# Optimization experiments

Hardware: AMD Instinct MI355X
Metric: run time of the kernel (lower is better)

Reference implementation:

```python
import jax, jax.numpy as jnp
import numpy as np

B, T, C, H, D = 2, 2048, 1024, 16, 64

def setup_inputs() -> dict:
    key = jax.random.key(0)
    ks = jax.random.split(key, 5)
    s = 1.0 / np.sqrt(C)
    return {
        "hidden_states": jax.random.normal(ks[0], (B, T, C), jnp.float32),
        "Wq": jax.random.normal(ks[1], (H, C, D), jnp.float32) * s,
        "Wk": jax.random.normal(ks[2], (H, C, D), jnp.float32) * s,
        "Wv": jax.random.normal(ks[3], (H, C, D), jnp.float32) * s,
        "Wo": jax.random.normal(ks[4], (C, C), jnp.float32) * s,
    }

def reference(hidden_states, Wq, Wk, Wv, Wo):
    x = hidden_states  # (B, T, C)
    q = jnp.einsum("btc,hcd->bhtd", x, Wq)
    k = jnp.einsum("btc,hcd->bhtd", x, Wk)
    v = jnp.einsum("btc,hcd->bhtd", x, Wv)
    scale = 1.0 / jnp.sqrt(jnp.asarray(D, x.dtype))
    scores = jnp.einsum("bhtd,bhsd->bhts", q, k) * scale  # (B,H,T,T)
    Tlen = x.shape[1]
    causal = jnp.tril(jnp.ones((Tlen, Tlen), bool))
    scores = jnp.where(causal, scores, jnp.asarray(-jnp.inf, x.dtype))
    probs = jax.nn.softmax(scores, axis=-1)
    heads = jnp.einsum("bhts,bhsd->bhtd", probs, v)  # (B,H,T,D)
    concat = heads.transpose(0, 2, 1, 3).reshape(x.shape[0], Tlen, H * D)  # (B,T,C)
    return jnp.einsum("btc,oc->bto", concat, Wo)  # output projection (dropout=0)
```

## Files before the change

kernel.cpp:

```cpp
#include <hip/hip_runtime.h>
#include <math.h>

#define B_ 2
#define T_ 2048
#define C_ 1024
#define H_ 16
#define D_ 64

typedef short short8 __attribute__((ext_vector_type(8)));
typedef float f32x4 __attribute__((ext_vector_type(4)));

#define LOG2E 1.44269504088896f

__device__ __forceinline__ unsigned short f2bf(float f) {
    unsigned int u = __float_as_uint(f);
    u += 0x7FFFu + ((u >> 16) & 1u);
    return (unsigned short)(u >> 16);
}

#define NCAST 2560

__global__ __launch_bounds__(256) void prep_all(
    const float* __restrict__ x,  const float* __restrict__ Wq,
    const float* __restrict__ Wk, const float* __restrict__ Wv,
    const float* __restrict__ Wo,
    unsigned short* __restrict__ xb,   unsigned short* __restrict__ Wall,
    unsigned short* __restrict__ wob,  int nX, int nW)
{
    const int bid = blockIdx.x;
    const int tid = threadIdx.x;
    if (bid < NCAST) {
        int i = (bid * 256 + tid) * 8;
        const float* s;
        unsigned short* d;
        if (i < nX) { s = x + i; d = xb + i; }
        else {
            int j = i - nX;
            if (j >= nW) return;
            s = Wo + j; d = wob + j;
        }
        float4 a = *(const float4*)s;
        float4 b = *(const float4*)(s + 4);
        ushort4 o0, o1;
        o0.x = f2bf(a.x); o0.y = f2bf(a.y); o0.z = f2bf(a.z); o0.w = f2bf(a.w);
        o1.x = f2bf(b.x); o1.y = f2bf(b.y); o1.z = f2bf(b.z); o1.w = f2bf(b.w);
        *(ushort4*)d = o0;
        *(ushort4*)(d + 4) = o1;
        return;
    }
    __shared__ float t[64][65];
    const int tb = bid - NCAST;
    const int c0 = (tb & 15) * 64;
    const int h  = (tb >> 4) & 15;
    const int z  = tb >> 8;
    const float* W = (z == 0) ? Wq : (z == 1) ? Wk : Wv;
    unsigned short* Wt = Wall + (size_t)z * H_ * D_ * C_;
    const int r = tid >> 4, c4 = (tid & 15) * 4;
    #pragma unroll
    for (int p = 0; p < 4; p++) {
        int cl = r + p * 16;
        float4 v = *(const float4*)&W[((size_t)h * C_ + c0 + cl) * D_ + c4];
        t[cl][c4 + 0] = v.x; t[cl][c4 + 1] = v.y;
        t[cl][c4 + 2] = v.z; t[cl][c4 + 3] = v.w;
    }
    __syncthreads();
    #pragma unroll
    for (int p = 0; p < 4; p++) {
        int d = r + p * 16;
        ushort4 o;
        o.x = f2bf(t[c4 + 0][d]); o.y = f2bf(t[c4 + 1][d]);
        o.z = f2bf(t[c4 + 2][d]); o.w = f2bf(t[c4 + 3][d]);
        *(ushort4*)&Wt[((size_t)h * D_ + d) * C_ + c0 + c4] = o;
    }
}

__global__ __launch_bounds__(256) void qkv_big(
    const unsigned short* __restrict__ X,
    const unsigned short* __restrict__ Wall,
    unsigned short* __restrict__ Qo,
    unsigned short* __restrict__ Ko,
    unsigned short* __restrict__ Vt)
{
    __shared__ unsigned short As[128][72];
    __shared__ unsigned short Bs[128][72];

    const int m0 = blockIdx.x * 128;
    const int n0 = blockIdx.y * 128;
    const int z  = n0 >> 10;
    const int tid = threadIdx.x;
    const int w = tid >> 6, lane = tid & 63, quad = lane >> 4, l16 = lane & 15;
    const int wm = w & 1, wn = w >> 1;
    const int lrow = tid >> 3, lcol = (tid & 7) * 8;

    f32x4 acc[4][4] = {};

    short8 ar[4], br[4];
    #pragma unroll
    for (int p = 0; p < 4; p++) {
        int r = lrow + p * 32;
        ar[p] = *(const short8*)&X[(size_t)(m0 + r) * C_ + lcol];
        br[p] = *(const short8*)&Wall[(size_t)(n0 + r) * C_ + lcol];
    }

    for (int k0 = 0; k0 < C_; k0 += 64) {
        __syncthreads();
        #pragma unroll
        for (int p = 0; p < 4; p++) {
            int r = lrow + p * 32;
            *(short8*)&As[r][lcol] = ar[p];
            *(short8*)&Bs[r][lcol] = br[p];
        }
        __syncthreads();
        if (k0 + 64 < C_) {
            #pragma unroll
            for (int p = 0; p < 4; p++) {
                int r = lrow + p * 32;
                ar[p] = *(const short8*)&X[(size_t)(m0 + r) * C_ + k0 + 64 + lcol];
                br[p] = *(const short8*)&Wall[(size_t)(n0 + r) * C_ + k0 + 64 + lcol];
            }
        }
        #pragma unroll
        for (int ks = 0; ks < 2; ks++) {
            short8 af[4], bf[4];
            #pragma unroll
            for (int i = 0; i < 4; i++)
                af[i] = *(const short8*)&As[wm * 64 + i * 16 + l16][ks * 32 + quad * 8];
            #pragma unroll
            for (int j = 0; j < 4; j++)
                bf[j] = *(const short8*)&Bs[wn * 64 + j * 16 + l16][ks * 32 + quad * 8];
            #pragma unroll
            for (int i = 0; i < 4; i++)
                #pragma unroll
                for (int j = 0; j < 4; j++)
                    acc[i][j] = __builtin_amdgcn_mfma_f32_16x16x32_bf16(af[i], bf[j], acc[i][j], 0, 0, 0);
        }
    }

    if (z == 2) {
        #pragma unroll
        for (int j = 0; j < 4; j++) {
            const int n = n0 + wn * 64 + j * 16 + l16;
            const int h = (n >> 6) & 15, d = n & 63;
            #pragma unroll
            for (int i = 0; i < 4; i++) {
                const int m = m0 + wm * 64 + i * 16 + quad * 4;
                const int b = m >> 11, t = m & (T_ - 1);
                ushort4 pk;
                pk.x = f2bf(acc[i][j][0]);
                pk.y = f2bf(acc[i][j][1]);
                pk.z = f2bf(acc[i][j][2]);
                pk.w = f2bf(acc[i][j][3]);
                *(ushort4*)&Vt[(((size_t)b * H_ + h) * D_ + d) * T_ + t] = pk;
            }
        }
    } else {
        const float scale = (z == 0) ? 0.125f * LOG2E : 1.0f;
        unsigned short* O = (z == 0) ? Qo : Ko;
        #pragma unroll
        for (int j = 0; j < 4; j++) {
            const int n = n0 + wn * 64 + j * 16 + l16;
            const int h = (n >> 6) & 15, d = n & 63;
            #pragma unroll
            for (int i = 0; i < 4; i++)
                #pragma unroll
                for (int r = 0; r < 4; r++) {
                    const int m = m0 + wm * 64 + i * 16 + quad * 4 + r;
                    const int b = m >> 11, t = m & (T_ - 1);
                    O[(((size_t)b * H_ + h) * T_ + t) * D_ + d] = f2bf(acc[i][j][r] * scale);
                }
        }
    }
}

__global__ __launch_bounds__(256, 4) void flash_mfma(
    const unsigned short* __restrict__ Q,
    const unsigned short* __restrict__ K,
    const unsigned short* __restrict__ Vt,
    unsigned short* __restrict__ CC)
{
    __shared__ unsigned short kst[64][72];
    __shared__ unsigned short vts[64][72];
    __shared__ unsigned short ps [64][72];
    __shared__ float flb[64];

    const int dd = blockIdx.x;
    const int W  = (dd & 7) * 128 + (dd >> 3);
    const int qb = W & 31;
    const int head = W >> 5;
    const int h = head & 15, b = head >> 4;

    const int tid = threadIdx.x;
    const int w = tid >> 6, lane = tid & 63, quad = lane >> 4, l16 = lane & 15;
    const int lrow = tid >> 3, lcol = (tid & 7) * 8;
    const size_t hb  = ((size_t)b * H_ + h) * T_;
    const size_t hbD = ((size_t)b * H_ + h) * D_;
    const int q0 = qb * 64;
    const int nkb = qb + 1;

    short8 qf[2];
    #pragma unroll
    for (int ks = 0; ks < 2; ks++)
        qf[ks] = *(const short8*)&Q[(hb + q0 + w * 16 + l16) * D_ + ks * 32 + quad * 8];

    float l_lane = 0.0f;
    f32x4 o[4] = {};

    short8 kreg[2], vreg[2];
    #pragma unroll
    for (int p = 0; p < 2; p++) {
        int r = lrow + p * 32;
        kreg[p] = *(const short8*)&K[(hb + r) * D_ + lcol];
        vreg[p] = *(const short8*)&Vt[(hbD + r) * T_ + lcol];
    }

    for (int kb = 0; kb < nkb; kb++) {
        __syncthreads();
        #pragma unroll
        for (int p = 0; p < 2; p++) {
            int r = lrow + p * 32;
            *(short8*)&kst[r][lcol] = kreg[p];
            *(short8*)&vts[r][lcol] = vreg[p];
        }
        __syncthreads();
        if (kb + 1 < nkb) {
            const int k0n = (kb + 1) * 64;
            #pragma unroll
            for (int p = 0; p < 2; p++) {
                int r = lrow + p * 32;
                kreg[p] = *(const short8*)&K[(hb + k0n + r) * D_ + lcol];
                vreg[p] = *(const short8*)&Vt[(hbD + r) * T_ + k0n + lcol];
            }
        }

        f32x4 s[4] = {};
        __builtin_amdgcn_s_setprio(1);
        #pragma unroll
        for (int ks = 0; ks < 2; ks++)
            #pragma unroll
            for (int ct = 0; ct < 4; ct++) {
                short8 kf = *(const short8*)&kst[ct * 16 + l16][ks * 32 + quad * 8];
                s[ct] = __builtin_amdgcn_mfma_f32_16x16x32_bf16(kf, qf[ks], s[ct], 0, 0, 0);
            }
        __builtin_amdgcn_s_setprio(0);

        if (kb == qb) {
            #pragma unroll
            for (int ct = 0; ct < 4; ct++)
                #pragma unroll
                for (int r = 0; r < 4; r++)
                    if (ct * 16 + quad * 4 + r > w * 16 + l16) s[ct][r] = -INFINITY;
        }

        #pragma unroll
        for (int ct = 0; ct < 4; ct++) {
            float e0 = exp2f(s[ct][0]);
            float e1 = exp2f(s[ct][1]);
            float e2 = exp2f(s[ct][2]);
            float e3 = exp2f(s[ct][3]);
            l_lane += (e0 + e1) + (e2 + e3);
            uint2 pk;
            pk.x = __builtin_amdgcn_perm(
                __float_as_uint(e1) + 0x8000u, __float_as_uint(e0) + 0x8000u, 0x07060302u);
            pk.y = __builtin_amdgcn_perm(
                __float_as_uint(e3) + 0x8000u, __float_as_uint(e2) + 0x8000u, 0x07060302u);
            *(uint2*)&ps[w * 16 + l16][ct * 16 + quad * 4] = pk;
        }

        __builtin_amdgcn_s_setprio(1);
        #pragma unroll
        for (int ks = 0; ks < 2; ks++) {
            short8 pa = *(const short8*)&ps[w * 16 + l16][ks * 32 + quad * 8];
            #pragma unroll
            for (int ct = 0; ct < 4; ct++) {
                short8 vf = *(const short8*)&vts[ct * 16 + l16][ks * 32 + quad * 8];
                o[ct] = __builtin_amdgcn_mfma_f32_16x16x32_bf16(pa, vf, o[ct], 0, 0, 0);
            }
        }
        __builtin_amdgcn_s_setprio(0);
    }

    l_lane += __shfl_xor(l_lane, 16);
    l_lane += __shfl_xor(l_lane, 32);
    if (lane < 16) flb[w * 16 + lane] = l_lane;
    #pragma unroll
    for (int r = 0; r < 4; r++) {
        const int q = w * 16 + quad * 4 + r;
        const float invl = 1.0f / flb[q];
        const int t = q0 + q;
        #pragma unroll
        for (int ct = 0; ct < 4; ct++)
            CC[((size_t)b * T_ + t) * C_ + h * D_ + ct * 16 + l16] = f2bf(o[ct][r] * invl);
    }
}

__global__ __launch_bounds__(256) void out_big(
    const unsigned short* __restrict__ X,
    const unsigned short* __restrict__ Wob,
    float* __restrict__ out)
{
    __shared__ unsigned short As[128][72];
    __shared__ unsigned short Bs[128][72];

    const int m0 = blockIdx.x * 128;
    const int n0 = blockIdx.y * 128;
    const int tid = threadIdx.x;
    const int w = tid >> 6, lane = tid & 63, quad = lane >> 4, l16 = lane & 15;
    const int wm = w & 1, wn = w >> 1;
    const int lrow = tid >> 3, lcol = (tid & 7) * 8;

    f32x4 acc[4][4] = {};

    short8 ar[4], br[4];
    #pragma unroll
    for (int p = 0; p < 4; p++) {
        int r = lrow + p * 32;
        ar[p] = *(const short8*)&X[(size_t)(m0 + r) * C_ + lcol];
        br[p] = *(const short8*)&Wob[(size_t)(n0 + r) * C_ + lcol];
    }

    for (int k0 = 0; k0 < C_; k0 += 64) {
        __syncthreads();
        #pragma unroll
        for (int p = 0; p < 4; p++) {
            int r = lrow + p * 32;
            *(short8*)&As[r][lcol] = ar[p];
            *(short8*)&Bs[r][lcol] = br[p];
        }
        __syncthreads();
        if (k0 + 64 < C_) {
            #pragma unroll
            for (int p = 0; p < 4; p++) {
                int r = lrow + p * 32;
                ar[p] = *(const short8*)&X[(size_t)(m0 + r) * C_ + k0 + 64 + lcol];
                br[p] = *(const short8*)&Wob[(size_t)(n0 + r) * C_ + k0 + 64 + lcol];
            }
        }
        #pragma unroll
        for (int ks = 0; ks < 2; ks++) {
            short8 af[4], bf[4];
            #pragma unroll
            for (int i = 0; i < 4; i++)
                af[i] = *(const short8*)&As[wm * 64 + i * 16 + l16][ks * 32 + quad * 8];
            #pragma unroll
            for (int j = 0; j < 4; j++)
                bf[j] = *(const short8*)&Bs[wn * 64 + j * 16 + l16][ks * 32 + quad * 8];
            #pragma unroll
            for (int i = 0; i < 4; i++)
                #pragma unroll
                for (int j = 0; j < 4; j++)
                    acc[i][j] = __builtin_amdgcn_mfma_f32_16x16x32_bf16(af[i], bf[j], acc[i][j], 0, 0, 0);
        }
    }

    #pragma unroll
    for (int i = 0; i < 4; i++)
        #pragma unroll
        for (int j = 0; j < 4; j++)
            #pragma unroll
            for (int r = 0; r < 4; r++)
                out[(size_t)(m0 + wm * 64 + i * 16 + quad * 4 + r) * C_ + n0 + wn * 64 + j * 16 + l16] = acc[i][j][r];
}

extern "C" void kernel_launch(void* const* d_in, const int* in_sizes, int n_in,
                              void* d_out, int out_size, void* d_ws, size_t ws_size,
                              hipStream_t stream) {
    const float* x  = (const float*)d_in[0];
    const float* Wq = (const float*)d_in[1];
    const float* Wk = (const float*)d_in[2];
    const float* Wv = (const float*)d_in[3];
    const float* Wo = (const float*)d_in[4];
    float* out = (float*)d_out;

    const size_t nX = (size_t)B_ * T_ * C_;
    const size_t nW = (size_t)H_ * C_ * D_;
    const size_t nQ = (size_t)B_ * H_ * T_ * D_;
    unsigned short* xb   = (unsigned short*)d_ws;
    unsigned short* Wall = xb + nX;
    unsigned short* Wob  = Wall + 3 * nW;
    unsigned short* Qb   = Wob + nW;
    unsigned short* Kb   = Qb + nQ;
    unsigned short* Vtb  = Kb + nQ;
    unsigned short* CCb  = Vtb + nQ;

    prep_all<<<dim3(NCAST + 768), 256, 0, stream>>>(
        x, Wq, Wk, Wv, Wo, xb, Wall, Wob, (int)nX, (int)nW);
    qkv_big<<<dim3(32, 24), 256, 0, stream>>>(xb, Wall, Qb, Kb, Vtb);
    flash_mfma<<<dim3(1024), 256, 0, stream>>>(Qb, Kb, Vtb, CCb);
    out_big<<<dim3(32, 8), 256, 0, stream>>>(CCb, Wob, out);
}
```

Baseline: 196.4 us.

## Pair complementary causal query blocks per workgroup to balance work and share K/V tiles

Each 512-thread workgroup now handles two query blocks of the same head, p and 31-p. Two groups of four waves share the K/V tiles staged in LDS, and the loop runs over the longer block's key range, with each group skipping tiles past its own causal limit. This balances causal work across workgroups, halves the grid, and halves K/V staging loads per query block. The cost is that the short-block group idles at barriers while the long block finishes, and occupancy per CU changes with the larger workgroups.

```diff
diff --git a/kernel.cpp b/kernel.cpp
--- a/kernel.cpp
+++ b/kernel.cpp
@@ -172,7 +172,7 @@
     }
 }
 
-__global__ __launch_bounds__(256, 4) void flash_mfma(
+__global__ __launch_bounds__(512, 4) void flash_mfma(
     const unsigned short* __restrict__ Q,
     const unsigned short* __restrict__ K,
     const unsigned short* __restrict__ Vt,
@@ -180,112 +180,110 @@
 {
     __shared__ unsigned short kst[64][72];
     __shared__ unsigned short vts[64][72];
-    __shared__ unsigned short ps [64][72];
-    __shared__ float flb[64];
-
-    const int dd = blockIdx.x;
-    const int W  = (dd & 7) * 128 + (dd >> 3);
-    const int qb = W & 31;
-    const int head = W >> 5;
+    __shared__ unsigned short ps [2][64][72];
+    __shared__ float flb[2][64];
+
+    const int d    = blockIdx.x;
+    const int x    = d & 7;
+    const int loc  = d >> 3;
+    const int half = loc >> 5, li = loc & 31;
+    const int hsub = li & 3, pr = li >> 2;
+    const int p    = half ? (15 - pr) : pr;
+    const int head = x * 4 + hsub;
     const int h = head & 15, b = head >> 4;
 
     const int tid = threadIdx.x;
     const int w = tid >> 6, lane = tid & 63, quad = lane >> 4, l16 = lane & 15;
+    const int wg = w & 3;
+    const int g  = w >> 2;
     const int lrow = tid >> 3, lcol = (tid & 7) * 8;
     const size_t hb  = ((size_t)b * H_ + h) * T_;
     const size_t hbD = ((size_t)b * H_ + h) * D_;
-    const int q0 = qb * 64;
-    const int nkb = qb + 1;
+
+    const int qb  = g ? (31 - p) : p;
+    const int q0  = qb * 64;
+    const int myn = qb + 1;
+    const int nkb = 32 - p;
 
     short8 qf[2];
     #pragma unroll
     for (int ks = 0; ks < 2; ks++)
-        qf[ks] = *(const short8*)&Q[(hb + q0 + w * 16 + l16) * D_ + ks * 32 + quad * 8];
+        qf[ks] = *(const short8*)&Q[(hb + q0 + wg * 16 + l16) * D_ + ks * 32 + quad * 8];
 
     float l_lane = 0.0f;
     f32x4 o[4] = {};
 
-    short8 kreg[2], vreg[2];
-    #pragma unroll
-    for (int p = 0; p < 2; p++) {
-        int r = lrow + p * 32;
-        kreg[p] = *(const short8*)&K[(hb + r) * D_ + lcol];
-        vreg[p] = *(const short8*)&Vt[(hbD + r) * T_ + lcol];
-    }
+    short8 kreg, vreg;
+    kreg = *(const short8*)&K[(hb + lrow) * D_ + lcol];
+    vreg = *(const short8*)&Vt[(hbD + lrow) * T_ + lcol];
 
     for (int kb = 0; kb < nkb; kb++) {
         __syncthreads();
-        #pragma unroll
-        for (int p = 0; p < 2; p++) {
-            int r = lrow + p * 32;
-            *(short8*)&kst[r][lcol] = kreg[p];
-            *(short8*)&vts[r][lcol] = vreg[p];
-        }
+        *(short8*)&kst[lrow][lcol] = kreg;
+        *(short8*)&vts[lrow][lcol] = vreg;
         __syncthreads();
         if (kb + 1 < nkb) {
             const int k0n = (kb + 1) * 64;
-            #pragma unroll
-            for (int p = 0; p < 2; p++) {
-                int r = lrow + p * 32;
-                kreg[p] = *(const short8*)&K[(hb + k0n + r) * D_ + lcol];
-                vreg[p] = *(const short8*)&Vt[(hbD + r) * T_ + k0n + lcol];
-            }
-        }
-
-        f32x4 s[4] = {};
-        __builtin_amdgcn_s_setprio(1);
-        #pragma unroll
-        for (int ks = 0; ks < 2; ks++)
+            kreg = *(const short8*)&K[(hb + k0n + lrow) * D_ + lcol];
+            vreg = *(const short8*)&Vt[(hbD + lrow) * T_ + k0n + lcol];
+        }
+
+        if (kb < myn) {
+            f32x4 s[4] = {};
+            __builtin_amdgcn_s_setprio(1);
+            #pragma unroll
+            for (int ks = 0; ks < 2; ks++)
+                #pragma unroll
+                for (int ct = 0; ct < 4; ct++) {
+                    short8 kf = *(const short8*)&kst[ct * 16 + l16][ks * 32 + quad * 8];
+                    s[ct] = __builtin_amdgcn_mfma_f32_16x16x32_bf16(kf, qf[ks], s[ct], 0, 0, 0);
+                }
+            __builtin_amdgcn_s_setprio(0);
+
+            if (kb == qb) {
+                #pragma unroll
+                for (int ct = 0; ct < 4; ct++)
+                    #pragma unroll
+                    for (int r = 0; r < 4; r++)
+                        if (ct * 16 + quad * 4 + r > wg * 16 + l16) s[ct][r] = -INFINITY;
+            }
+
             #pragma unroll
             for (int ct = 0; ct < 4; ct++) {
-                short8 kf = *(const short8*)&kst[ct * 16 + l16][ks * 32 + quad * 8];
-                s[ct] = __builtin_amdgcn_mfma_f32_16x16x32_bf16(kf, qf[ks], s[ct], 0, 0, 0);
-            }
-        __builtin_amdgcn_s_setprio(0);
-
-        if (kb == qb) {
-            #pragma unroll
-            for (int ct = 0; ct < 4; ct++)
-                #pragma unroll
-                for (int r = 0; r < 4; r++)
-                    if (ct * 16 + quad * 4 + r > w * 16 + l16) s[ct][r] = -INFINITY;
-        }
-
-        #pragma unroll
-        for (int ct = 0; ct < 4; ct++) {
-            float e0 = exp2f(s[ct][0]);
-            float e1 = exp2f(s[ct][1]);
-            float e2 = exp2f(s[ct][2]);
-            float e3 = exp2f(s[ct][3]);
-            l_lane += (e0 + e1) + (e2 + e3);
-            uint2 pk;
-            pk.x = __builtin_amdgcn_perm(
-                __float_as_uint(e1) + 0x8000u, __float_as_uint(e0) + 0x8000u, 0x07060302u);
-            pk.y = __builtin_amdgcn_perm(
-                __float_as_uint(e3) + 0x8000u, __float_as_uint(e2) + 0x8000u, 0x07060302u);
-            *(uint2*)&ps[w * 16 + l16][ct * 16 + quad * 4] = pk;
-        }
-
-        __builtin_amdgcn_s_setprio(1);
-        #pragma unroll
-        for (int ks = 0; ks < 2; ks++) {
-            short8 pa = *(const short8*)&ps[w * 16 + l16][ks * 32 + quad * 8];
-            #pragma unroll
-            for (int ct = 0; ct < 4; ct++) {
-                short8 vf = *(const short8*)&vts[ct * 16 + l16][ks * 32 + quad * 8];
-                o[ct] = __builtin_amdgcn_mfma_f32_16x16x32_bf16(pa, vf, o[ct], 0, 0, 0);
-            }
-        }
-        __builtin_amdgcn_s_setprio(0);
+                float e0 = exp2f(s[ct][0]);
+                float e1 = exp2f(s[ct][1]);
+                float e2 = exp2f(s[ct][2]);
+                float e3 = exp2f(s[ct][3]);
+                l_lane += (e0 + e1) + (e2 + e3);
+                uint2 pk;
+                pk.x = __builtin_amdgcn_perm(
+                    __float_as_uint(e1) + 0x8000u, __float_as_uint(e0) + 0x8000u, 0x07060302u);
+                pk.y = __builtin_amdgcn_perm(
+                    __float_as_uint(e3) + 0x8000u, __float_as_uint(e2) + 0x8000u, 0x07060302u);
+                *(uint2*)&ps[g][wg * 16 + l16][ct * 16 + quad * 4] = pk;
+            }
+
+            __builtin_amdgcn_s_setprio(1);
+            #pragma unroll
+            for (int ks = 0; ks < 2; ks++) {
+                short8 pa = *(const short8*)&ps[g][wg * 16 + l16][ks * 32 + quad * 8];
+                #pragma unroll
+                for (int ct = 0; ct < 4; ct++) {
+                    short8 vf = *(const short8*)&vts[ct * 16 + l16][ks * 32 + quad * 8];
+                    o[ct] = __builtin_amdgcn_mfma_f32_16x16x32_bf16(pa, vf, o[ct], 0, 0, 0);
+                }
+            }
+            __builtin_amdgcn_s_setprio(0);
+        }
     }
 
     l_lane += __shfl_xor(l_lane, 16);
     l_lane += __shfl_xor(l_lane, 32);
-    if (lane < 16) flb[w * 16 + lane] = l_lane;
+    if (lane < 16) flb[g][wg * 16 + lane] = l_lane;
     #pragma unroll
     for (int r = 0; r < 4; r++) {
-        const int q = w * 16 + quad * 4 + r;
-        const float invl = 1.0f / flb[q];
+        const int q = wg * 16 + quad * 4 + r;
+        const float invl = 1.0f / flb[g][q];
         const int t = q0 + q;
         #pragma unroll
         for (int ct = 0; ct < 4; ct++)
@@ -385,6 +383,6 @@
     prep_all<<<dim3(NCAST + 768), 256, 0, stream>>>(
         x, Wq, Wk, Wv, Wo, xb, Wall, Wob, (int)nX, (int)nW);
     qkv_big<<<dim3(32, 24), 256, 0, stream>>>(xb, Wall, Qb, Kb, Vtb);
-    flash_mfma<<<dim3(1024), 256, 0, stream>>>(Qb, Kb, Vtb, CCb);
+    flash_mfma<<<dim3(512), 512, 0, stream>>>(Qb, Kb, Vtb, CCb);
     out_big<<<dim3(32, 8), 256, 0, stream>>>(CCb, Wob, out);
 }
```

Measured after the change: 174.8 us. 1.12x faster.
